# Kernel optimization log

Hardware: AMD Instinct MI355X
Metric: run time of the kernel (lower is better)

## Reference

```python
import jax, jax.numpy as jnp
import numpy as np

B, L, D_MODEL, H = 4, 2048, 1024, 16
HD = D_MODEL // H  # head_dim = 64


def _rope_tables(seq_len, dim, dtype):
    inv_freq = 1.0 / (10000.0 ** (jnp.arange(0, dim, 2, dtype=jnp.float32) / dim))
    t = jnp.arange(seq_len, dtype=jnp.float32)
    freqs = jnp.outer(t, inv_freq)  # (S, dim/2)
    return jnp.cos(freqs).astype(dtype), jnp.sin(freqs).astype(dtype)


def _apply_rope(x):
    # x: (B, H, S, d)
    cos, sin = _rope_tables(x.shape[-2], x.shape[-1], x.dtype)  # (S, d/2)
    x_even = x[..., 0::2]
    x_odd = x[..., 1::2]
    out_even = x_even * cos - x_odd * sin
    out_odd = x_even * sin + x_odd * cos
    return jnp.stack([out_even, out_odd], axis=-1).reshape(x.shape)


def setup_inputs() -> dict:
    key = jax.random.key(0)
    ks = jax.random.split(key, 9)
    s = 1.0 / np.sqrt(D_MODEL)
    inp = {
        "query": jax.random.normal(ks[0], (B, L, D_MODEL), dtype=jnp.float32),
        "Wq": jax.random.uniform(ks[1], (D_MODEL, D_MODEL), jnp.float32, -s, s),
        "bq": jax.random.uniform(ks[2], (D_MODEL,), jnp.float32, -s, s),
        "Wk": jax.random.uniform(ks[3], (D_MODEL, D_MODEL), jnp.float32, -s, s),
        "bk": jax.random.uniform(ks[4], (D_MODEL,), jnp.float32, -s, s),
        "Wv": jax.random.uniform(ks[5], (D_MODEL, D_MODEL), jnp.float32, -s, s),
        "bv": jax.random.uniform(ks[6], (D_MODEL,), jnp.float32, -s, s),
        "Wo": jax.random.uniform(ks[7], (D_MODEL, D_MODEL), jnp.float32, -s, s),
        "bo": jax.random.uniform(ks[8], (D_MODEL,), jnp.float32, -s, s),
    }
    return inp


def reference(query, Wq, bq, Wk, bk, Wv, bv, Wo, bo):
    Bq, Lq, _ = query.shape
    # projections (torch Linear: x @ W.T + b), split into heads -> (B, H, L, d)
    def proj(x, W, b):
        y = x @ W.T + b
        return y.reshape(Bq, Lq, H, HD).transpose(0, 2, 1, 3)
    q = _apply_rope(proj(query, Wq, bq))
    k = _apply_rope(proj(query, Wk, bk))
    v = proj(query, Wv, bv)
    scores = jnp.einsum("bhqd,bhkd->bhqk", q, k) / np.sqrt(HD)
    causal_mask = jnp.triu(jnp.ones((Lq, Lq), dtype=bool), k=1)
    scores = jnp.where(causal_mask[None, None, :, :], -jnp.inf, scores)
    attn = jax.nn.softmax(scores, axis=-1)
    out = jnp.einsum("bhqk,bhkd->bhqd", attn, v)
    out = out.transpose(0, 2, 1, 3).reshape(Bq, Lq, D_MODEL)
    return out @ Wo.T + bo
```

## Files before the change

kernel.cpp:

```cpp
#include <hip/hip_runtime.h>
#include <hip/hip_bf16.h>
#include <math.h>

#define L_SEQ  2048
#define DMODEL 1024
#define NHEAD  16
#define HEADD  64

typedef __attribute__((ext_vector_type(8))) short short8;
typedef __attribute__((ext_vector_type(4))) short short4v;
typedef __attribute__((ext_vector_type(4))) float f32x4;

static __device__ __forceinline__ unsigned short f2bf(float f) {
    unsigned int u = __float_as_uint(f);
    unsigned int r = (u + 0x7fffu + ((u >> 16) & 1u)) >> 16;
    return (unsigned short)r;
}

static __device__ __forceinline__ void dma16(const unsigned short* g, unsigned short* l) {
    __builtin_amdgcn_global_load_lds((const __attribute__((address_space(1))) void*)g,
                                     (__attribute__((address_space(3))) void*)l, 16, 0, 0);
}

__global__ void cvt_f32_bf16(const float* __restrict__ in,
                             unsigned short* __restrict__ out, int n4) {
    int i = blockIdx.x * blockDim.x + threadIdx.x;
    if (i >= n4) return;
    float4 v = reinterpret_cast<const float4*>(in)[i];
    ushort4 o;
    o.x = f2bf(v.x); o.y = f2bf(v.y); o.z = f2bf(v.z); o.w = f2bf(v.w);
    reinterpret_cast<ushort4*>(out)[i] = o;
}

__global__ void cvt_weights(const float* __restrict__ Wq, const float* __restrict__ Wk,
                            const float* __restrict__ Wv, const float* __restrict__ Wo,
                            unsigned short* __restrict__ dst) {
    int i = blockIdx.x * blockDim.x + threadIdx.x;
    int which = i >> 18;
    const float* src = which == 0 ? Wq : which == 1 ? Wk : which == 2 ? Wv : Wo;
    float4 v = reinterpret_cast<const float4*>(src)[i & 262143];
    ushort4 o;
    o.x = f2bf(v.x); o.y = f2bf(v.y); o.z = f2bf(v.z); o.w = f2bf(v.w);
    reinterpret_cast<ushort4*>(dst)[i] = o;
}

__global__ void build_rope(float* __restrict__ tab) {
    int i = blockIdx.x * blockDim.x + threadIdx.x;
    int lpos = i >> 5, i2 = i & 31;
    float inv_f = expf(-0.28782313662425574f * (float)i2);
    float ang = (float)lpos * inv_f;
    tab[2 * i]     = cosf(ang);
    tab[2 * i + 1] = sinf(ang);
}

#define BKP 32

__global__ __launch_bounds__(256) void proj_qkv(
    const unsigned short* __restrict__ X,
    const unsigned short* __restrict__ Wqkv,
    const float* __restrict__ bq_,
    const float* __restrict__ bk_,
    const float* __restrict__ bv_,
    const float* __restrict__ rope,
    unsigned short* __restrict__ Qb,
    unsigned short* __restrict__ Kb,
    unsigned short* __restrict__ Vr)
{
    __shared__ unsigned short pool[24576];
    unsigned short* a_ring = pool;
    unsigned short* b_ring = pool + 12288;

    const int tid  = threadIdx.x;
    const int lane = tid & 63;
    const int w    = tid >> 6;
    const int wm   = w & 1, wn = w >> 1;
    const int quad = lane >> 4, l16 = lane & 15;

    const int orig = blockIdx.y * 24 + blockIdx.x;
    const int swz  = (orig & 7) * 192 + (orig >> 3);
    const int bx   = swz % 24;
    const int by   = swz / 24;
    const int m0   = by * 128;
    const int n0   = bx * 128;

    const int sel = bx >> 3;
    const float* bias   = sel == 0 ? bq_ : (sel == 1 ? bk_ : bv_);
    unsigned short* out = sel == 0 ? Qb  : (sel == 1 ? Kb  : Vr);

    const int st_row = lane >> 2;
    const int st_col = (((lane & 3) ^ ((lane >> 3) & 3)) << 3);
    const int rd = ((quad ^ ((l16 >> 1) & 3)) << 3);

    f32x4 acc[4][4];
#pragma unroll
    for (int i = 0; i < 4; ++i)
#pragma unroll
        for (int j = 0; j < 4; ++j) acc[i][j] = (f32x4){0.f, 0.f, 0.f, 0.f};

    const unsigned short* Xs = X    + (size_t)(m0 + w * 32 + st_row) * DMODEL + st_col;
    const unsigned short* Ws = Wqkv + (size_t)(n0 + w * 32 + st_row) * DMODEL + st_col;
    const int ldsA0 = (w * 32) * BKP, ldsA1 = (w * 32 + 16) * BKP;

#pragma unroll
    for (int p = 0; p < 2; ++p) {
        const int kk = p * BKP;
        dma16(Xs + kk,               a_ring + p * 4096 + ldsA0);
        dma16(Xs + 16 * DMODEL + kk, a_ring + p * 4096 + ldsA1);
        dma16(Ws + kk,               b_ring + p * 4096 + ldsA0);
        dma16(Ws + 16 * DMODEL + kk, b_ring + p * 4096 + ldsA1);
    }
    asm volatile("s_waitcnt vmcnt(4)" ::: "memory");
    __builtin_amdgcn_s_barrier();

    for (int kt = 0; kt < 32; ++kt) {
        const int slot = (kt % 3) * 4096;
        const int ps   = ((kt + 2) % 3) * 4096;
        const int kk   = ((kt + 2) & 31) * BKP;

        short8 af[4], bf[2];
#pragma unroll
        for (int i = 0; i < 4; ++i)
            af[i] = *reinterpret_cast<const short8*>(
                &a_ring[slot + (wm * 64 + i * 16 + l16) * BKP + rd]);
#pragma unroll
        for (int j = 0; j < 2; ++j)
            bf[j] = *reinterpret_cast<const short8*>(
                &b_ring[slot + (wn * 64 + j * 16 + l16) * BKP + rd]);
        dma16(Xs + kk,               a_ring + ps + ldsA0);
        dma16(Xs + 16 * DMODEL + kk, a_ring + ps + ldsA1);
        __builtin_amdgcn_s_barrier();
        asm volatile("s_waitcnt lgkmcnt(0)" ::: "memory");
        __builtin_amdgcn_sched_barrier(0);
        __builtin_amdgcn_s_setprio(1);
#pragma unroll
        for (int i = 0; i < 4; ++i)
#pragma unroll
            for (int j = 0; j < 2; ++j)
                acc[i][j] = __builtin_amdgcn_mfma_f32_16x16x32_bf16(af[i], bf[j], acc[i][j], 0, 0, 0);
        __builtin_amdgcn_s_setprio(0);
        __builtin_amdgcn_s_barrier();

#pragma unroll
        for (int j = 0; j < 2; ++j)
            bf[j] = *reinterpret_cast<const short8*>(
                &b_ring[slot + (wn * 64 + (2 + j) * 16 + l16) * BKP + rd]);
        dma16(Ws + kk,               b_ring + ps + ldsA0);
        dma16(Ws + 16 * DMODEL + kk, b_ring + ps + ldsA1);
        __builtin_amdgcn_s_barrier();
        asm volatile("s_waitcnt lgkmcnt(0)" ::: "memory");
        __builtin_amdgcn_sched_barrier(0);
        __builtin_amdgcn_s_setprio(1);
#pragma unroll
        for (int i = 0; i < 4; ++i)
#pragma unroll
            for (int j = 0; j < 2; ++j)
                acc[i][2 + j] = __builtin_amdgcn_mfma_f32_16x16x32_bf16(af[i], bf[j], acc[i][2 + j], 0, 0, 0);
        __builtin_amdgcn_s_setprio(0);
        asm volatile("s_waitcnt vmcnt(4)" ::: "memory");
        __builtin_amdgcn_s_barrier();
    }
    asm volatile("s_waitcnt vmcnt(0)" ::: "memory");
    __builtin_amdgcn_s_barrier();

#pragma unroll
    for (int jf = 0; jf < 4; ++jf) {
        int nl = wn * 64 + jf * 16 + l16;
        int nn = (bx & 7) * 128 + nl;
        float bval = bias[nn];
        int d  = nn & (HEADD - 1);
        float sgn = (d & 1) ? 1.0f : -1.0f;
        int i2 = d >> 1;
#pragma unroll
        for (int mf = 0; mf < 4; ++mf) {
#pragma unroll
            for (int r = 0; r < 4; ++r) {
                int ml = wm * 64 + mf * 16 + quad * 4 + r;
                int lpos = (m0 + ml) & (L_SEQ - 1);
                float v = acc[mf][jf][r] + bval;
                if (sel < 2) {
                    float p = __shfl_xor(v, 1);
                    float2 cs = *reinterpret_cast<const float2*>(&rope[(size_t)(lpos * 32 + i2) * 2]);
                    v = v * cs.x + sgn * cs.y * p;
                    if (sel == 0) v *= 0.18033688011112042f;
                }
                pool[(sel < 2) ? (ml * 136 + nl) : (nl * 136 + ml)] = f2bf(v);
            }
        }
    }
    __builtin_amdgcn_s_barrier();

    const int b     = m0 >> 11;
    const int lpos0 = m0 & (L_SEQ - 1);
#pragma unroll
    for (int i = 0; i < 8; ++i) {
        int g   = i * 256 + tid;
        int row = g >> 4;
        int c8  = (g & 15) * 8;
        int4 val = *reinterpret_cast<const int4*>(&pool[row * 136 + c8]);
        size_t addr;
        if (sel < 2) {
            int n_g = (bx & 7) * 128 + c8;
            int h = n_g >> 6, d = n_g & 63;
            addr = ((size_t)(b * NHEAD + h) * L_SEQ + (lpos0 + row)) * HEADD + d;
        } else {
            int n_g = (bx & 7) * 128 + row;
            int h = n_g >> 6, d = n_g & 63;
            addr = ((size_t)(b * NHEAD + h) * HEADD + d) * L_SEQ + lpos0 + c8;
        }
        *reinterpret_cast<int4*>(out + addr) = val;
    }
}

__global__ __launch_bounds__(256) void attn_fwd(
    const unsigned short* __restrict__ Q,
    const unsigned short* __restrict__ K,
    const unsigned short* __restrict__ Vt,
    unsigned short* __restrict__ Oa)
{
    __shared__ unsigned short k_lds[2][64 * 64];
    __shared__ unsigned short v_lds[2][64 * 64];
    const int tid  = threadIdx.x;
    const int lane = tid & 63;
    const int w    = tid >> 6;
    const int quad = lane >> 4, l16 = lane & 15;
    const int pair = blockIdx.y;
    const int bh   = blockIdx.x;
    const size_t base = (size_t)bh * L_SEQ * HEADD;
    const int b = bh >> 4, h = bh & 15;

    const int srow  = lane >> 3;
    const int sslot = lane & 7;
    const int ssw   = ((sslot ^ srow) << 3);
    const unsigned short* Ksrc = K  + base + (size_t)(w * 8 + srow) * HEADD  + ssw;
    const unsigned short* Vsrc = Vt + base + (size_t)(w * 8 + srow) * L_SEQ + ssw;
    const int d0 = (w * 8) * 64;
    const int d1 = (32 + w * 8) * 64;
    const int swr = (l16 & 7);

    for (int half = 0; half < 2; ++half) {
        const int qb = half ? (31 - pair) : pair;
        const int qrow = qb * 64 + w * 16 + l16;

        short8 qf[2];
#pragma unroll
        for (int ks = 0; ks < 2; ++ks)
            qf[ks] = *reinterpret_cast<const short8*>(Q + base + (size_t)qrow * HEADD + ks * 32 + quad * 8);

        f32x4 o[4];
#pragma unroll
        for (int nt = 0; nt < 4; ++nt) o[nt] = (f32x4){0.f, 0.f, 0.f, 0.f};
        float lsum = 0.f;

        dma16(Ksrc,                 &k_lds[0][d0]);
        dma16(Ksrc + 32 * HEADD,    &k_lds[0][d1]);
        dma16(Vsrc,                 &v_lds[0][d0]);
        dma16(Vsrc + 32 * L_SEQ,    &v_lds[0][d1]);
        asm volatile("s_waitcnt vmcnt(0)" ::: "memory");
        __builtin_amdgcn_s_barrier();

        int cur = 0;
        for (int kb = 0; kb <= qb; ++kb) {
            const int kn = (kb + 1) <= qb ? (kb + 1) : 0;
            const int nb = cur ^ 1;
            dma16(Ksrc + (size_t)(kn * 64) * HEADD,        &k_lds[nb][d0]);
            dma16(Ksrc + (size_t)(kn * 64 + 32) * HEADD,   &k_lds[nb][d1]);
            dma16(Vsrc + kn * 64,                          &v_lds[nb][d0]);
            dma16(Vsrc + kn * 64 + 32 * L_SEQ,             &v_lds[nb][d1]);

            f32x4 st[4];
#pragma unroll
            for (int nt = 0; nt < 4; ++nt) st[nt] = (f32x4){0.f, 0.f, 0.f, 0.f};
            __builtin_amdgcn_s_setprio(1);
#pragma unroll
            for (int ks = 0; ks < 2; ++ks)
#pragma unroll
                for (int nt = 0; nt < 4; ++nt) {
                    short8 kf = *reinterpret_cast<const short8*>(
                        &k_lds[cur][(nt * 16 + l16) * 64 + (((ks * 4 + quad) ^ swr) << 3)]);
                    st[nt] = __builtin_amdgcn_mfma_f32_16x16x32_bf16(kf, qf[ks], st[nt], 0, 0, 0);
                }
            __builtin_amdgcn_s_setprio(0);

            if (kb == qb) {
#pragma unroll
                for (int nt = 0; nt < 4; ++nt)
#pragma unroll
                    for (int r = 0; r < 4; ++r) {
                        int seqcol = kb * 64 + nt * 16 + quad * 4 + r;
                        if (seqcol > qrow) st[nt][r] = -INFINITY;
                    }
            }

            short4v pfrag[4];
#pragma unroll
            for (int nt = 0; nt < 4; ++nt) {
                float p0 = __builtin_amdgcn_exp2f(st[nt][0]);
                float p1 = __builtin_amdgcn_exp2f(st[nt][1]);
                float p2 = __builtin_amdgcn_exp2f(st[nt][2]);
                float p3 = __builtin_amdgcn_exp2f(st[nt][3]);
                lsum += (p0 + p1) + (p2 + p3);
                unsigned u0 = __float_as_uint(p0) + 0x8000u;
                unsigned u1 = __float_as_uint(p1) + 0x8000u;
                unsigned u2 = __float_as_uint(p2) + 0x8000u;
                unsigned u3 = __float_as_uint(p3) + 0x8000u;
                union { unsigned u[2]; short4v v; } pk;
                pk.u[0] = (u0 >> 16) | (u1 & 0xffff0000u);
                pk.u[1] = (u2 >> 16) | (u3 & 0xffff0000u);
                pfrag[nt] = pk.v;
            }

            __builtin_amdgcn_s_setprio(1);
#pragma unroll
            for (int c = 0; c < 4; ++c)
#pragma unroll
                for (int nt2 = 0; nt2 < 4; ++nt2) {
                    short4v vf = *reinterpret_cast<const short4v*>(
                        &v_lds[cur][(nt2 * 16 + l16) * 64 +
                                    (((c * 2 + (quad >> 1)) ^ swr) << 3) + ((quad & 1) << 2)]);
                    o[nt2] = __builtin_amdgcn_mfma_f32_16x16x16bf16_1k(pfrag[c], vf, o[nt2], 0, 0, 0);
                }
            __builtin_amdgcn_s_setprio(0);

            asm volatile("s_waitcnt vmcnt(0)" ::: "memory");
            __builtin_amdgcn_s_barrier();
            cur ^= 1;
        }

        lsum += __shfl_xor(lsum, 16);
        lsum += __shfl_xor(lsum, 32);
        float rs[4];
#pragma unroll
        for (int r = 0; r < 4; ++r) rs[r] = __shfl(lsum, quad * 4 + r);
#pragma unroll
        for (int r = 0; r < 4; ++r) {
            float inv = 1.0f / rs[r];
            int lg = qb * 64 + w * 16 + quad * 4 + r;
#pragma unroll
            for (int nt = 0; nt < 4; ++nt) {
                int d = nt * 16 + l16;
                Oa[(size_t)(b * L_SEQ + lg) * DMODEL + h * HEADD + d] = f2bf(o[nt][r] * inv);
            }
        }
    }
}

#define LDA 32

__global__ __launch_bounds__(256) void out_gemm(
    const unsigned short* __restrict__ X,
    const unsigned short* __restrict__ W,
    const float* __restrict__ bias,
    float* __restrict__ out)
{
    __shared__ unsigned short a_lds[3][128 * BKP];
    __shared__ unsigned short b_lds[3][128 * BKP];
    const int tid  = threadIdx.x;
    const int lane = tid & 63;
    const int w    = tid >> 6;
    const int wm   = w & 1, wn = w >> 1;
    const int quad = lane >> 4, l16 = lane & 15;

    const int orig = blockIdx.y * 8 + blockIdx.x;
    const int swz  = (orig & 7) * 64 + (orig >> 3);
    const int m0 = (swz >> 3) * 128;
    const int n0 = (swz & 7) * 128;

    const int st_row = lane >> 2;
    const int st_col = (((lane & 3) ^ ((lane >> 3) & 3)) << 3);
    const int rd = ((quad ^ ((l16 >> 1) & 3)) << 3);

    f32x4 acc[4][4];
#pragma unroll
    for (int i = 0; i < 4; ++i)
#pragma unroll
        for (int j = 0; j < 4; ++j) acc[i][j] = (f32x4){0.f, 0.f, 0.f, 0.f};

    const unsigned short* Xs = X + (size_t)(m0 + w * 32 + st_row) * DMODEL + st_col;
    const unsigned short* Ws = W + (size_t)(n0 + w * 32 + st_row) * DMODEL + st_col;
    const int ldsA0 = (w * 32) * BKP, ldsA1 = (w * 32 + 16) * BKP;

#pragma unroll
    for (int p = 0; p < 2; ++p) {
        const int kk = p * BKP;
        dma16(Xs + kk,               &a_lds[p][ldsA0]);
        dma16(Xs + 16 * DMODEL + kk, &a_lds[p][ldsA1]);
        dma16(Ws + kk,               &b_lds[p][ldsA0]);
        dma16(Ws + 16 * DMODEL + kk, &b_lds[p][ldsA1]);
    }
    asm volatile("s_waitcnt vmcnt(4)" ::: "memory");
    __builtin_amdgcn_s_barrier();

    for (int kt = 0; kt < 32; ++kt) {
        const int slot = kt % 3;
        const int ps   = (kt + 2) % 3;
        const int kk   = ((kt + 2) & 31) * BKP;

        dma16(Xs + kk,               &a_lds[ps][ldsA0]);
        dma16(Xs + 16 * DMODEL + kk, &a_lds[ps][ldsA1]);
        dma16(Ws + kk,               &b_lds[ps][ldsA0]);
        dma16(Ws + 16 * DMODEL + kk, &b_lds[ps][ldsA1]);

        short8 af[4], bf[4];
#pragma unroll
        for (int i = 0; i < 4; ++i)
            af[i] = *reinterpret_cast<const short8*>(
                &a_lds[slot][(wm * 64 + i * 16 + l16) * BKP + rd]);
#pragma unroll
        for (int j = 0; j < 4; ++j)
            bf[j] = *reinterpret_cast<const short8*>(
                &b_lds[slot][(wn * 64 + j * 16 + l16) * BKP + rd]);
        asm volatile("s_waitcnt lgkmcnt(0)" ::: "memory");
        __builtin_amdgcn_sched_barrier(0);
        __builtin_amdgcn_s_setprio(1);
#pragma unroll
        for (int i = 0; i < 4; ++i)
#pragma unroll
            for (int j = 0; j < 4; ++j)
                acc[i][j] = __builtin_amdgcn_mfma_f32_16x16x32_bf16(af[i], bf[j], acc[i][j], 0, 0, 0);
        __builtin_amdgcn_s_setprio(0);
        asm volatile("s_waitcnt vmcnt(4)" ::: "memory");
        __builtin_amdgcn_s_barrier();
    }
    asm volatile("s_waitcnt vmcnt(0)" ::: "memory");

#pragma unroll
    for (int nt = 0; nt < 4; ++nt) {
        int n_g = n0 + wn * 64 + nt * 16 + l16;
        float bv = bias[n_g];
#pragma unroll
        for (int mt = 0; mt < 4; ++mt)
#pragma unroll
            for (int r = 0; r < 4; ++r) {
                int m_g = m0 + wm * 64 + mt * 16 + quad * 4 + r;
                out[(size_t)m_g * DMODEL + n_g] = acc[mt][nt][r] + bv;
            }
    }
}

extern "C" void kernel_launch(void* const* d_in, const int* in_sizes, int n_in,
                              void* d_out, int out_size, void* d_ws, size_t ws_size,
                              hipStream_t stream) {
    const float* query = (const float*)d_in[0];
    const float* Wq = (const float*)d_in[1];
    const float* bq = (const float*)d_in[2];
    const float* Wk = (const float*)d_in[3];
    const float* bk = (const float*)d_in[4];
    const float* Wv = (const float*)d_in[5];
    const float* bv = (const float*)d_in[6];
    const float* Wo = (const float*)d_in[7];
    const float* bo = (const float*)d_in[8];
    float* out = (float*)d_out;

    unsigned short* ws  = (unsigned short*)d_ws;
    unsigned short* xb  = ws;
    unsigned short* wqb = xb  + (size_t)8388608;
    unsigned short* wkb = wqb + 1048576;
    unsigned short* wvb = wkb + 1048576;
    unsigned short* wob = wvb + 1048576;
    unsigned short* Qb  = wob + 1048576;
    unsigned short* Kb  = Qb  + 8388608;
    unsigned short* Vr  = Kb  + 8388608;
    unsigned short* Ab  = Vr  + 8388608;
    float* rope = (float*)(Ab + 8388608);

    (void)wkb; (void)wvb;

    build_rope<<<256, 256, 0, stream>>>(rope);
    cvt_f32_bf16<<<8192, 256, 0, stream>>>(query, xb, 2097152);
    cvt_weights<<<4096, 256, 0, stream>>>(Wq, Wk, Wv, Wo, wqb);

    proj_qkv<<<dim3(24, 64), 256, 0, stream>>>(xb, wqb, bq, bk, bv, rope, Qb, Kb, Vr);
    attn_fwd<<<dim3(64, 16), 256, 0, stream>>>(Qb, Kb, Vr, Ab);
    out_gemm<<<dim3(8, 64), 256, 0, stream>>>(Ab, wob, bo, out);
}
```

Measured before the change: 288.3 us.

## Process two query tiles per attention block to reuse K/V loads

Each attention block now handles a 128-row query strip as two 64-row tiles that share every K/V tile loaded into LDS, and the grid's second dimension is halved. This raises MFMA work per LDS load and per barrier, cutting K/V traffic per query row. In exchange it doubles accumulator registers, may lower occupancy, computes a fully masked extra key block for the first tile, and leaves fewer blocks to balance the causal workload.

Result: no change. 283.8 us (-1.5%).

```diff
diff --git a/kernel.cpp b/kernel.cpp
--- a/kernel.cpp
+++ b/kernel.cpp
@@ -231,25 +231,32 @@
     const int srow  = lane >> 3;
     const int sslot = lane & 7;
     const int ssw   = ((sslot ^ srow) << 3);
-    const unsigned short* Ksrc = K  + base + (size_t)(w * 8 + srow) * HEADD  + ssw;
+    const unsigned short* Ksrc = K  + base + (size_t)(w * 8 + srow) * HEADD + ssw;
     const unsigned short* Vsrc = Vt + base + (size_t)(w * 8 + srow) * L_SEQ + ssw;
     const int d0 = (w * 8) * 64;
     const int d1 = (32 + w * 8) * 64;
     const int swr = (l16 & 7);
 
     for (int half = 0; half < 2; ++half) {
-        const int qb = half ? (31 - pair) : pair;
-        const int qrow = qb * 64 + w * 16 + l16;
-
-        short8 qf[2];
-#pragma unroll
-        for (int ks = 0; ks < 2; ++ks)
-            qf[ks] = *reinterpret_cast<const short8*>(Q + base + (size_t)qrow * HEADD + ks * 32 + quad * 8);
-
-        f32x4 o[4];
-#pragma unroll
-        for (int nt = 0; nt < 4; ++nt) o[nt] = (f32x4){0.f, 0.f, 0.f, 0.f};
-        float lsum = 0.f;
+        const int s = half ? (15 - pair) : pair;
+        const int qrow0 = s * 128 + w * 16 + l16;
+        const int qrow1 = qrow0 + 64;
+        const int kbmax = 2 * s + 1;
+
+        short8 qf0[2], qf1[2];
+#pragma unroll
+        for (int ks = 0; ks < 2; ++ks) {
+            qf0[ks] = *reinterpret_cast<const short8*>(Q + base + (size_t)qrow0 * HEADD + ks * 32 + quad * 8);
+            qf1[ks] = *reinterpret_cast<const short8*>(Q + base + (size_t)qrow1 * HEADD + ks * 32 + quad * 8);
+        }
+
+        f32x4 o0[4], o1[4];
+#pragma unroll
+        for (int nt = 0; nt < 4; ++nt) {
+            o0[nt] = (f32x4){0.f, 0.f, 0.f, 0.f};
+            o1[nt] = (f32x4){0.f, 0.f, 0.f, 0.f};
+        }
+        float lsum0 = 0.f, lsum1 = 0.f;
 
         dma16(Ksrc,                 &k_lds[0][d0]);
         dma16(Ksrc + 32 * HEADD,    &k_lds[0][d1]);
@@ -259,17 +266,20 @@
         __builtin_amdgcn_s_barrier();
 
         int cur = 0;
-        for (int kb = 0; kb <= qb; ++kb) {
-            const int kn = (kb + 1) <= qb ? (kb + 1) : 0;
+        for (int kb = 0; kb <= kbmax; ++kb) {
+            const int kn = (kb + 1) <= kbmax ? (kb + 1) : 0;
             const int nb = cur ^ 1;
             dma16(Ksrc + (size_t)(kn * 64) * HEADD,        &k_lds[nb][d0]);
             dma16(Ksrc + (size_t)(kn * 64 + 32) * HEADD,   &k_lds[nb][d1]);
             dma16(Vsrc + kn * 64,                          &v_lds[nb][d0]);
             dma16(Vsrc + kn * 64 + 32 * L_SEQ,             &v_lds[nb][d1]);
 
-            f32x4 st[4];
-#pragma unroll
-            for (int nt = 0; nt < 4; ++nt) st[nt] = (f32x4){0.f, 0.f, 0.f, 0.f};
+            f32x4 st0[4], st1[4];
+#pragma unroll
+            for (int nt = 0; nt < 4; ++nt) {
+                st0[nt] = (f32x4){0.f, 0.f, 0.f, 0.f};
+                st1[nt] = (f32x4){0.f, 0.f, 0.f, 0.f};
+            }
             __builtin_amdgcn_s_setprio(1);
 #pragma unroll
             for (int ks = 0; ks < 2; ++ks)
@@ -277,28 +287,38 @@
                 for (int nt = 0; nt < 4; ++nt) {
                     short8 kf = *reinterpret_cast<const short8*>(
                         &k_lds[cur][(nt * 16 + l16) * 64 + (((ks * 4 + quad) ^ swr) << 3)]);
-                    st[nt] = __builtin_amdgcn_mfma_f32_16x16x32_bf16(kf, qf[ks], st[nt], 0, 0, 0);
+                    st0[nt] = __builtin_amdgcn_mfma_f32_16x16x32_bf16(kf, qf0[ks], st0[nt], 0, 0, 0);
+                    st1[nt] = __builtin_amdgcn_mfma_f32_16x16x32_bf16(kf, qf1[ks], st1[nt], 0, 0, 0);
                 }
             __builtin_amdgcn_s_setprio(0);
 
-            if (kb == qb) {
+            if (kb >= 2 * s) {
 #pragma unroll
                 for (int nt = 0; nt < 4; ++nt)
 #pragma unroll
                     for (int r = 0; r < 4; ++r) {
                         int seqcol = kb * 64 + nt * 16 + quad * 4 + r;
-                        if (seqcol > qrow) st[nt][r] = -INFINITY;
+                        if (seqcol > qrow0) st0[nt][r] = -INFINITY;
                     }
             }
-
-            short4v pfrag[4];
+            if (kb == kbmax) {
+#pragma unroll
+                for (int nt = 0; nt < 4; ++nt)
+#pragma unroll
+                    for (int r = 0; r < 4; ++r) {
+                        int seqcol = kb * 64 + nt * 16 + quad * 4 + r;
+                        if (seqcol > qrow1) st1[nt][r] = -INFINITY;
+                    }
+            }
+
+            short4v pfrag0[4], pfrag1[4];
 #pragma unroll
             for (int nt = 0; nt < 4; ++nt) {
-                float p0 = __builtin_amdgcn_exp2f(st[nt][0]);
-                float p1 = __builtin_amdgcn_exp2f(st[nt][1]);
-                float p2 = __builtin_amdgcn_exp2f(st[nt][2]);
-                float p3 = __builtin_amdgcn_exp2f(st[nt][3]);
-                lsum += (p0 + p1) + (p2 + p3);
+                float p0 = __builtin_amdgcn_exp2f(st0[nt][0]);
+                float p1 = __builtin_amdgcn_exp2f(st0[nt][1]);
+                float p2 = __builtin_amdgcn_exp2f(st0[nt][2]);
+                float p3 = __builtin_amdgcn_exp2f(st0[nt][3]);
+                lsum0 += (p0 + p1) + (p2 + p3);
                 unsigned u0 = __float_as_uint(p0) + 0x8000u;
                 unsigned u1 = __float_as_uint(p1) + 0x8000u;
                 unsigned u2 = __float_as_uint(p2) + 0x8000u;
@@ -306,7 +326,21 @@
                 union { unsigned u[2]; short4v v; } pk;
                 pk.u[0] = (u0 >> 16) | (u1 & 0xffff0000u);
                 pk.u[1] = (u2 >> 16) | (u3 & 0xffff0000u);
-                pfrag[nt] = pk.v;
+                pfrag0[nt] = pk.v;
+
+                float q0e = __builtin_amdgcn_exp2f(st1[nt][0]);
+                float q1e = __builtin_amdgcn_exp2f(st1[nt][1]);
+                float q2e = __builtin_amdgcn_exp2f(st1[nt][2]);
+                float q3e = __builtin_amdgcn_exp2f(st1[nt][3]);
+                lsum1 += (q0e + q1e) + (q2e + q3e);
+                unsigned v0 = __float_as_uint(q0e) + 0x8000u;
+                unsigned v1 = __float_as_uint(q1e) + 0x8000u;
+                unsigned v2 = __float_as_uint(q2e) + 0x8000u;
+                unsigned v3 = __float_as_uint(q3e) + 0x8000u;
+                union { unsigned u[2]; short4v v; } pk1;
+                pk1.u[0] = (v0 >> 16) | (v1 & 0xffff0000u);
+                pk1.u[1] = (v2 >> 16) | (v3 & 0xffff0000u);
+                pfrag1[nt] = pk1.v;
             }
 
             __builtin_amdgcn_s_setprio(1);
@@ -317,7 +351,8 @@
                     short4v vf = *reinterpret_cast<const short4v*>(
                         &v_lds[cur][(nt2 * 16 + l16) * 64 +
                                     (((c * 2 + (quad >> 1)) ^ swr) << 3) + ((quad & 1) << 2)]);
-                    o[nt2] = __builtin_amdgcn_mfma_f32_16x16x16bf16_1k(pfrag[c], vf, o[nt2], 0, 0, 0);
+                    o0[nt2] = __builtin_amdgcn_mfma_f32_16x16x16bf16_1k(pfrag0[c], vf, o0[nt2], 0, 0, 0);
+                    o1[nt2] = __builtin_amdgcn_mfma_f32_16x16x16bf16_1k(pfrag1[c], vf, o1[nt2], 0, 0, 0);
                 }
             __builtin_amdgcn_s_setprio(0);
 
@@ -326,25 +361,31 @@
             cur ^= 1;
         }
 
-        lsum += __shfl_xor(lsum, 16);
-        lsum += __shfl_xor(lsum, 32);
-        float rs[4];
-#pragma unroll
-        for (int r = 0; r < 4; ++r) rs[r] = __shfl(lsum, quad * 4 + r);
+        lsum0 += __shfl_xor(lsum0, 16);
+        lsum0 += __shfl_xor(lsum0, 32);
+        lsum1 += __shfl_xor(lsum1, 16);
+        lsum1 += __shfl_xor(lsum1, 32);
+        float rs0[4], rs1[4];
 #pragma unroll
         for (int r = 0; r < 4; ++r) {
-            float inv = 1.0f / rs[r];
-            int lg = qb * 64 + w * 16 + quad * 4 + r;
+            rs0[r] = __shfl(lsum0, quad * 4 + r);
+            rs1[r] = __shfl(lsum1, quad * 4 + r);
+        }
+#pragma unroll
+        for (int r = 0; r < 4; ++r) {
+            float inv0 = 1.0f / rs0[r];
+            float inv1 = 1.0f / rs1[r];
+            int lg0 = s * 128 + w * 16 + quad * 4 + r;
+            int lg1 = lg0 + 64;
 #pragma unroll
             for (int nt = 0; nt < 4; ++nt) {
                 int d = nt * 16 + l16;
-                Oa[(size_t)(b * L_SEQ + lg) * DMODEL + h * HEADD + d] = f2bf(o[nt][r] * inv);
-            }
-        }
-    }
-}
-
-#define LDA 32
+                Oa[(size_t)(b * L_SEQ + lg0) * DMODEL + h * HEADD + d] = f2bf(o0[nt][r] * inv0);
+                Oa[(size_t)(b * L_SEQ + lg1) * DMODEL + h * HEADD + d] = f2bf(o1[nt][r] * inv1);
+            }
+        }
+    }
+}
 
 __global__ __launch_bounds__(256) void out_gemm(
     const unsigned short* __restrict__ X,
@@ -470,6 +511,6 @@
     cvt_weights<<<4096, 256, 0, stream>>>(Wq, Wk, Wv, Wo, wqb);
 
     proj_qkv<<<dim3(24, 64), 256, 0, stream>>>(xb, wqb, bq, bk, bv, rope, Qb, Kb, Vr);
-    attn_fwd<<<dim3(64, 16), 256, 0, stream>>>(Qb, Kb, Vr, Ab);
+    attn_fwd<<<dim3(64, 8), 256, 0, stream>>>(Qb, Kb, Vr, Ab);
     out_gemm<<<dim3(8, 64), 256, 0, stream>>>(Ab, wob, bo, out);
 }
```
